# Kernel optimization log

Hardware: AMD Instinct MI355X
Metric: run time of the kernel (lower is better)

Reference implementation:

```python
import jax, jax.numpy as jnp
import numpy as np

B, M, H, E, V, U = 1024, 15, 256, 256, 30000, 1000


def setup_inputs() -> dict:
    key = jax.random.key(0)
    ks = jax.random.split(key, 24)
    s = 0.05  # weight init scale
    return {
        "input_ids": jax.random.randint(ks[0], (B, 1), 0, V),
        "input_embedding": jax.random.normal(ks[1], (B, 1, E), jnp.float32),
        "hidden": jax.random.normal(ks[2], (1, B, H), jnp.float32),
        "inter_output": jax.random.normal(ks[3], (B, M, H), jnp.float32),
        "user_list": jax.random.randint(ks[4], (B,), 0, U),
        # per-user parameter tables (torch ModuleLists of Linear); stored [in,out]
        "inter_W": jax.random.normal(ks[5], (U, H, H), jnp.float32) * s,
        "inter_b": jax.random.normal(ks[6], (U, H), jnp.float32) * s,
        "hidden_W": jax.random.normal(ks[7], (U, H, H), jnp.float32) * s,
        "hidden_b": jax.random.normal(ks[8], (U, H), jnp.float32) * s,
        "lt1_W": jax.random.normal(ks[9], (U, 2 * H, H), jnp.float32) * s,
        "lt1_b": jax.random.normal(ks[10], (U, H), jnp.float32) * s,
        "scale_W": jax.random.normal(ks[11], (U, H), jnp.float32) * s,
        "scale_b": jax.random.normal(ks[12], (U,), jnp.float32) * s,
        # GRU (1 layer), torch layout: W_ih [3H, 2E], W_hh [3H, H], gate order r,z,n
        "gru_Wih": jax.random.normal(ks[13], (3 * H, 2 * E), jnp.float32) * s,
        "gru_Whh": jax.random.normal(ks[14], (3 * H, H), jnp.float32) * s,
        "gru_bih": jax.random.normal(ks[15], (3 * H,), jnp.float32) * s,
        "gru_bhh": jax.random.normal(ks[16], (3 * H,), jnp.float32) * s,
        # output projection, stored [H, V]
        "lin_W": jax.random.normal(ks[17], (H, V), jnp.float32) * s,
        "lin_b": jax.random.normal(ks[18], (V,), jnp.float32) * s,
    }


def reference(input_ids, input_embedding, hidden, inter_output, user_list,
              inter_W, inter_b, hidden_W, hidden_b, lt1_W, lt1_b,
              scale_W, scale_b, gru_Wih, gru_Whh, gru_bih, gru_bhh,
              lin_W, lin_b):
    embedded_input = input_embedding  # dropout p=0 (eval)
    hidden_t = jnp.transpose(hidden, (1, 0, 2))  # [B,1,H]

    # per-user intra attention: gather user weights, batched GEMMs (replaces python loop)
    Wi = inter_W[user_list]                      # [B,H,H]
    inter_output_a = jnp.einsum('bmh,bho->bmo', inter_output, Wi) + inter_b[user_list][:, None, :]
    Wh = hidden_W[user_list]                     # [B,H,H]
    hidden_t_a = jnp.einsum('bih,bho->bio', hidden_t, Wh) + hidden_b[user_list][:, None, :]  # [B,1,H]
    cat = jnp.concatenate([jnp.broadcast_to(hidden_t_a, (hidden_t_a.shape[0], M, H)), inter_output_a], axis=2)  # [B,M,2H]
    result = jnp.tanh(jnp.einsum('bmk,bko->bmo', cat, lt1_W[user_list]) + lt1_b[user_list][:, None, :])  # [B,M,H]
    energies = jnp.einsum('bmh,bh->bm', result, scale_W[user_list]) + scale_b[user_list][:, None]  # [B,M]

    attn_weights = jax.nn.softmax(energies, axis=1)                      # [B,M]
    context = jnp.einsum('bm,bmh->bh', attn_weights, inter_output)[:, None, :]  # [B,1,H]

    gru_input = jnp.concatenate([embedded_input, context], axis=2)  # [B,1,2E]
    x = gru_input[:, 0, :]
    h = hidden[0]
    gi = x @ gru_Wih.T + gru_bih   # [B,3H]
    gh = h @ gru_Whh.T + gru_bhh
    gi_r, gi_z, gi_n = jnp.split(gi, 3, axis=1)
    gh_r, gh_z, gh_n = jnp.split(gh, 3, axis=1)
    r = jax.nn.sigmoid(gi_r + gh_r)
    z = jax.nn.sigmoid(gi_z + gh_z)
    n = jnp.tanh(gi_n + r * gh_n)
    h_new = (1.0 - z) * n + z * h
    gru_output = h_new[:, None, :]       # [B,1,H]
    hidden_new = h_new[None, :, :]       # [1,B,H]

    output = gru_output @ lin_W + lin_b  # [B,1,V]
    return (output, hidden_new, embedded_input, gru_output, attn_weights)
```

## Files before the change

### kernel.cpp

```cpp
#include <hip/hip_runtime.h>
#include <math.h>

#define B 1024
#define M 15
#define H 256
#define E 256
#define V 30000
#define U 1000

typedef float  vf4    __attribute__((ext_vector_type(4)));
typedef __bf16 bf16x8 __attribute__((ext_vector_type(8)));
typedef float  f32x4  __attribute__((ext_vector_type(4)));

#define O_OUT   0
#define O_HID   ((size_t)B*V)
#define O_EMB   (O_HID + (size_t)B*H)
#define O_GRU   (O_EMB + (size_t)B*E)
#define O_ATT   (O_GRU + (size_t)B*H)

#define GLDS(g, l) __builtin_amdgcn_global_load_lds( \
    (const __attribute__((address_space(1))) void*)(g), \
    (__attribute__((address_space(3))) void*)(l), 16, 0, 0)

union BF8 { __bf16 h[8]; bf16x8 v; };
union BF4 { __bf16 h[4]; unsigned long long u; };

__global__ __launch_bounds__(1024) void sort_kernel(
    const int* __restrict__ ul, int* __restrict__ order, int* __restrict__ rbase_g)
{
    __shared__ int cnt[1024];
    __shared__ int base[1024];
    const int tid = threadIdx.x;
    cnt[tid] = 0;
    __syncthreads();
    const int u = ul[tid];
    atomicAdd(&cnt[u], 1);
    __syncthreads();
    int c0 = cnt[tid];
    int v  = c0;
    for (int off = 1; off < 1024; off <<= 1) {
        int add = (tid >= off) ? cnt[tid - off] : 0;
        __syncthreads();
        v += add;
        cnt[tid] = v;
        __syncthreads();
    }
    base[tid]   = v - c0;
    rbase_g[tid] = v - c0;
    __syncthreads();
    int pos = atomicAdd(&base[u], 1);
    order[pos] = tid;
}

__global__ __launch_bounds__(256, 4) void attn_kernel(
    const float* __restrict__ hidden,
    const float* __restrict__ inter_output,
    const int*   __restrict__ user_list,
    const int*   __restrict__ order,
    const int*   __restrict__ rbase,
    const float* __restrict__ inter_W,
    const float* __restrict__ inter_b,
    const float* __restrict__ hidden_W,
    const float* __restrict__ hidden_b,
    const float* __restrict__ lt1_W,
    const float* __restrict__ lt1_b,
    const float* __restrict__ scale_W,
    const float* __restrict__ scale_b,
    float* __restrict__ out,
    __bf16* __restrict__ xcat)
{
    const int s   = ((blockIdx.x & 7) << 7) + (blockIdx.x >> 3);
    const int b0  = order[s];
    const int u   = user_list[b0];
    if ((s - rbase[u]) & 1) return;
    bool paired = false;
    int  b1 = b0;
    if (s + 1 < B) {
        int ob = order[s + 1];
        if (user_list[ob] == u) { paired = true; b1 = ob; }
    }

    const int tid  = threadIdx.x;
    const int lane = tid & 63;
    const int wave = tid >> 6;
    const int wn0  = wave * 64;

    __shared__ __align__(16) __bf16 Abuf[32 * 512];
    __shared__ __align__(16) __bf16 hta[2][256];
    __shared__ float red[2][64];
    __shared__ float e_lds[2][16];

    {
        const int r    = tid >> 3;
        const int part = tid & 7;
        const int sm   = r >> 4;
        const int mr   = r & 15;
        const int bs   = sm ? b1 : b0;
        const bool zr  = (sm == 1) && !paired;
        #pragma unroll
        for (int it = 0; it < 8; ++it) {
            int c = part + it * 8;
            int k = c * 8;
            BF8 p;
            #pragma unroll
            for (int j = 0; j < 8; ++j) p.h[j] = (__bf16)0.f;
            if (!zr) {
                if (mr < 15 && k < 256) {
                    vf4 f0 = *(const vf4*)&inter_output[(size_t)bs * M * H + mr * H + k];
                    vf4 f1 = *(const vf4*)&inter_output[(size_t)bs * M * H + mr * H + k + 4];
                    p.h[0]=(__bf16)f0[0]; p.h[1]=(__bf16)f0[1]; p.h[2]=(__bf16)f0[2]; p.h[3]=(__bf16)f0[3];
                    p.h[4]=(__bf16)f1[0]; p.h[5]=(__bf16)f1[1]; p.h[6]=(__bf16)f1[2]; p.h[7]=(__bf16)f1[3];
                } else if (mr == 15 && k >= 256) {
                    vf4 f0 = *(const vf4*)&hidden[(size_t)bs * H + (k - 256)];
                    vf4 f1 = *(const vf4*)&hidden[(size_t)bs * H + (k - 256) + 4];
                    p.h[0]=(__bf16)f0[0]; p.h[1]=(__bf16)f0[1]; p.h[2]=(__bf16)f0[2]; p.h[3]=(__bf16)f0[3];
                    p.h[4]=(__bf16)f1[0]; p.h[5]=(__bf16)f1[1]; p.h[6]=(__bf16)f1[2]; p.h[7]=(__bf16)f1[3];
                }
            }
            *(bf16x8*)&Abuf[r * 512 + (c ^ (r & 7)) * 8] = p.v;
        }
    }
    __syncthreads();

    const float* Wi_base  = inter_W  + (size_t)u * H * H;
    const float* Wh_base  = hidden_W + (size_t)u * H * H;
    const float* lt1_base = lt1_W    + (size_t)u * 2 * H * H;

    const int ocol = wn0 + (lane & 15);
    const int krow = (lane >> 4) * 8;

    f32x4 acc1[2][4];
    #pragma unroll
    for (int mf = 0; mf < 2; ++mf)
        #pragma unroll
        for (int nf = 0; nf < 4; ++nf) { f32x4 z = {0.f,0.f,0.f,0.f}; acc1[mf][nf] = z; }

    #pragma unroll 2
    for (int ks = 0; ks < 16; ++ks) {
        const float* Bp = ((ks < 8) ? (Wi_base + (size_t)(ks * 32) * H)
                                    : (Wh_base + (size_t)((ks - 8) * 32) * H))
                          + (size_t)krow * H + ocol;
        float t[4][8];
        #pragma unroll
        for (int j = 0; j < 8; ++j)
            #pragma unroll
            for (int nf = 0; nf < 4; ++nf)
                t[nf][j] = Bp[(size_t)j * H + nf * 16];
        bf16x8 bfr[4];
        #pragma unroll
        for (int nf = 0; nf < 4; ++nf) {
            BF8 pk;
            #pragma unroll
            for (int j = 0; j < 8; ++j) pk.h[j] = (__bf16)t[nf][j];
            bfr[nf] = pk.v;
        }
        int sca = ((ks * 4 + (lane >> 4)) ^ (lane & 7)) * 8;
        bf16x8 a0 = *(const bf16x8*)&Abuf[(lane & 15) * 512 + sca];
        #pragma unroll
        for (int nf = 0; nf < 4; ++nf)
            acc1[0][nf] = __builtin_amdgcn_mfma_f32_16x16x32_bf16(a0, bfr[nf], acc1[0][nf], 0, 0, 0);
        if (paired) {
            bf16x8 a1 = *(const bf16x8*)&Abuf[(16 + (lane & 15)) * 512 + sca];
            #pragma unroll
            for (int nf = 0; nf < 4; ++nf)
                acc1[1][nf] = __builtin_amdgcn_mfma_f32_16x16x32_bf16(a1, bfr[nf], acc1[1][nf], 0, 0, 0);
        }
    }
    __syncthreads();

    if ((lane >> 4) == 3) {
        #pragma unroll
        for (int nf = 0; nf < 4; ++nf) {
            int o = wn0 + nf * 16 + (lane & 15);
            float hb = hidden_b[(size_t)u * H + o];
            hta[0][o] = (__bf16)(acc1[0][nf][3] + hb);
            hta[1][o] = (__bf16)(acc1[1][nf][3] + hb);
        }
    }
    #pragma unroll
    for (int mf = 0; mf < 2; ++mf) {
        #pragma unroll
        for (int nf = 0; nf < 4; ++nf) {
            int o  = wn0 + nf * 16 + (lane & 15);
            float bi = inter_b[(size_t)u * H + o];
            int k  = 256 + o;
            #pragma unroll
            for (int j = 0; j < 4; ++j) {
                int r  = mf * 16 + (lane >> 4) * 4 + j;
                Abuf[r * 512 + ((k >> 3) ^ (r & 7)) * 8 + (k & 7)] = (__bf16)(acc1[mf][nf][j] + bi);
            }
        }
    }
    __syncthreads();

    {
        const int r    = tid >> 3;
        const int part = tid & 7;
        const int sm   = r >> 4;
        #pragma unroll
        for (int it = 0; it < 4; ++it) {
            int c = part + it * 8;
            bf16x8 hv = *(const bf16x8*)&hta[sm][c * 8];
            *(bf16x8*)&Abuf[r * 512 + (c ^ (r & 7)) * 8] = hv;
        }
    }
    __syncthreads();

    f32x4 acc2[2][4];
    #pragma unroll
    for (int mf = 0; mf < 2; ++mf)
        #pragma unroll
        for (int nf = 0; nf < 4; ++nf) { f32x4 z = {0.f,0.f,0.f,0.f}; acc2[mf][nf] = z; }

    #pragma unroll 2
    for (int ks = 0; ks < 16; ++ks) {
        const float* Bp = lt1_base + (size_t)(ks * 32) * H + (size_t)krow * H + ocol;
        float t[4][8];
        #pragma unroll
        for (int j = 0; j < 8; ++j)
            #pragma unroll
            for (int nf = 0; nf < 4; ++nf)
                t[nf][j] = Bp[(size_t)j * H + nf * 16];
        bf16x8 bfr[4];
        #pragma unroll
        for (int nf = 0; nf < 4; ++nf) {
            BF8 pk;
            #pragma unroll
            for (int j = 0; j < 8; ++j) pk.h[j] = (__bf16)t[nf][j];
            bfr[nf] = pk.v;
        }
        int sca = ((ks * 4 + (lane >> 4)) ^ (lane & 7)) * 8;
        bf16x8 a0 = *(const bf16x8*)&Abuf[(lane & 15) * 512 + sca];
        #pragma unroll
        for (int nf = 0; nf < 4; ++nf)
            acc2[0][nf] = __builtin_amdgcn_mfma_f32_16x16x32_bf16(a0, bfr[nf], acc2[0][nf], 0, 0, 0);
        if (paired) {
            bf16x8 a1 = *(const bf16x8*)&Abuf[(16 + (lane & 15)) * 512 + sca];
            #pragma unroll
            for (int nf = 0; nf < 4; ++nf)
                acc2[1][nf] = __builtin_amdgcn_mfma_f32_16x16x32_bf16(a1, bfr[nf], acc2[1][nf], 0, 0, 0);
        }
    }

    float p0[4] = {0.f,0.f,0.f,0.f};
    float p1[4] = {0.f,0.f,0.f,0.f};
    #pragma unroll
    for (int nf = 0; nf < 4; ++nf) {
        int o = wn0 + nf * 16 + (lane & 15);
        float l1b = lt1_b[(size_t)u * H + o];
        float sw  = scale_W[(size_t)u * H + o];
        #pragma unroll
        for (int j = 0; j < 4; ++j)
            p0[j] += tanhf(acc2[0][nf][j] + l1b) * sw;
        if (paired)
            #pragma unroll
            for (int j = 0; j < 4; ++j)
                p1[j] += tanhf(acc2[1][nf][j] + l1b) * sw;
    }
    #pragma unroll
    for (int j = 0; j < 4; ++j) {
        float v = p0[j];
        v += __shfl_xor(v, 1, 64); v += __shfl_xor(v, 2, 64);
        v += __shfl_xor(v, 4, 64); v += __shfl_xor(v, 8, 64);
        if ((lane & 15) == 0) red[0][wave * 16 + (lane >> 4) * 4 + j] = v;
        float w = p1[j];
        w += __shfl_xor(w, 1, 64); w += __shfl_xor(w, 2, 64);
        w += __shfl_xor(w, 4, 64); w += __shfl_xor(w, 8, 64);
        if ((lane & 15) == 0) red[1][wave * 16 + (lane >> 4) * 4 + j] = w;
    }
    __syncthreads();
    if (tid < 32) {
        int sm = tid >> 4, mm = tid & 15;
        e_lds[sm][mm] = red[sm][mm] + red[sm][16 + mm] + red[sm][32 + mm] + red[sm][48 + mm]
                      + scale_b[u];
    }
    __syncthreads();

    const int nsm = paired ? 2 : 1;
    for (int sm = 0; sm < nsm; ++sm) {
        const int bs = sm ? b1 : b0;
        float mx = -1e30f;
        #pragma unroll
        for (int m = 0; m < M; ++m) mx = fmaxf(mx, e_lds[sm][m]);
        float sum = 0.f;
        float aw[M];
        #pragma unroll
        for (int m = 0; m < M; ++m) { aw[m] = expf(e_lds[sm][m] - mx); sum += aw[m]; }
        float inv = 1.f / sum;
        if (tid < M) out[O_ATT + (size_t)bs * M + tid] = aw[tid] * inv;
        float ctx = 0.f;
        #pragma unroll
        for (int m = 0; m < M; ++m)
            ctx += aw[m] * inter_output[(size_t)bs * M * H + m * H + tid];
        xcat[(size_t)bs * 768 + 256 + tid] = (__bf16)(ctx * inv);
    }
}

__global__ __launch_bounds__(256) void cvt_xh_kernel(
    const float* __restrict__ emb, const float* __restrict__ hidden,
    __bf16* __restrict__ xcat, float* __restrict__ out)
{
    const int b = blockIdx.x, tid = threadIdx.x;
    float ev = emb[(size_t)b * E + tid];
    float hv = hidden[(size_t)b * H + tid];
    xcat[(size_t)b * 768 + tid]       = (__bf16)ev;
    xcat[(size_t)b * 768 + 512 + tid] = (__bf16)hv;
    out[O_EMB + (size_t)b * E + tid]  = ev;
}

__global__ __launch_bounds__(192) void wcat_kernel(
    const float* __restrict__ Wih, const float* __restrict__ Whh,
    __bf16* __restrict__ wcat)
{
    const int n = blockIdx.x;
    const int k = threadIdx.x * 4;
    vf4 v = {0.f, 0.f, 0.f, 0.f};
    if (n < 512) {
        v = (k < 512) ? *(const vf4*)&Wih[(size_t)n * 512 + k]
                      : *(const vf4*)&Whh[(size_t)n * 256 + (k - 512)];
    } else if (n < 768) {
        if (k < 512) v = *(const vf4*)&Wih[(size_t)n * 512 + k];
    } else {
        if (k >= 512) v = *(const vf4*)&Whh[(size_t)(n - 256) * 256 + (k - 512)];
    }
    BF4 p;
    p.h[0]=(__bf16)v[0]; p.h[1]=(__bf16)v[1]; p.h[2]=(__bf16)v[2]; p.h[3]=(__bf16)v[3];
    *(unsigned long long*)&wcat[(size_t)n * 768 + k] = p.u;
}

__global__ __launch_bounds__(256) void xgemm_kernel(
    const __bf16* __restrict__ xcat, const __bf16* __restrict__ wcat,
    float* __restrict__ gates)
{
    const int n0   = blockIdx.x * 256;
    const int m0   = blockIdx.y * 64;
    const int tid  = threadIdx.x;
    const int wave = tid >> 6, lane = tid & 63;
    const int wn0  = wave * 64;

    __shared__ __align__(16) __bf16 Al[64 * 64];
    __shared__ __align__(16) __bf16 Bl[256 * 64];

    f32x4 acc[4][4];
    #pragma unroll
    for (int mf = 0; mf < 4; ++mf)
        #pragma unroll
        for (int nf = 0; nf < 4; ++nf) { f32x4 z = {0.f,0.f,0.f,0.f}; acc[mf][nf] = z; }

    for (int ks = 0; ks < 12; ++ks) {
        #pragma unroll
        for (int r = 0; r < 2; ++r) {
            int L = r * 256 + tid;
            int m = L >> 3, c = L & 7;
            int sc = c ^ (m & 7);
            GLDS(xcat + (size_t)(m0 + m) * 768 + ks * 64 + sc * 8, &Al[(size_t)L * 8]);
        }
        #pragma unroll
        for (int r = 0; r < 8; ++r) {
            int L = r * 256 + tid;
            int n = L >> 3, c = L & 7;
            int sc = c ^ (n & 7);
            GLDS(wcat + (size_t)(n0 + n) * 768 + ks * 64 + sc * 8, &Bl[(size_t)L * 8]);
        }
        __syncthreads();
        #pragma unroll
        for (int kk = 0; kk < 2; ++kk) {
            bf16x8 af[4];
            #pragma unroll
            for (int mf = 0; mf < 4; ++mf) {
                int row = mf * 16 + (lane & 15);
                int c   = kk * 4 + (lane >> 4);
                af[mf] = *(const bf16x8*)&Al[row * 64 + (c ^ (row & 7)) * 8];
            }
            bf16x8 bfr[4];
            #pragma unroll
            for (int nf = 0; nf < 4; ++nf) {
                int col = wn0 + nf * 16 + (lane & 15);
                int c   = kk * 4 + (lane >> 4);
                bfr[nf] = *(const bf16x8*)&Bl[col * 64 + (c ^ (col & 7)) * 8];
            }
            #pragma unroll
            for (int mf = 0; mf < 4; ++mf)
                #pragma unroll
                for (int nf = 0; nf < 4; ++nf)
                    acc[mf][nf] = __builtin_amdgcn_mfma_f32_16x16x32_bf16(
                        af[mf], bfr[nf], acc[mf][nf], 0, 0, 0);
        }
        __syncthreads();
    }

    #pragma unroll
    for (int nf = 0; nf < 4; ++nf) {
        int n = n0 + wn0 + nf * 16 + (lane & 15);
        #pragma unroll
        for (int mf = 0; mf < 4; ++mf) {
            int rbase_ = m0 + mf * 16 + (lane >> 4) * 4;
            f32x4 a = acc[mf][nf];
            #pragma unroll
            for (int j = 0; j < 4; ++j)
                gates[(size_t)(rbase_ + j) * 1024 + n] = a[j];
        }
    }
}

__global__ __launch_bounds__(256) void gate_kernel(
    const float* __restrict__ gates,
    const float* __restrict__ hidden,
    const float* __restrict__ bih, const float* __restrict__ bhh,
    float* __restrict__ out, __bf16* __restrict__ hnb)
{
    const int b = blockIdx.x, j = threadIdx.x;
    const float* g = gates + (size_t)b * 1024;
    float rs  = g[j]       + bih[j]       + bhh[j];
    float zs  = g[256 + j] + bih[256 + j] + bhh[256 + j];
    float gin = g[512 + j] + bih[512 + j];
    float ghn = g[768 + j] + bhh[512 + j];
    float h   = hidden[(size_t)b * H + j];
    float r_  = 1.f / (1.f + expf(-rs));
    float z_  = 1.f / (1.f + expf(-zs));
    float n_  = tanhf(gin + r_ * ghn);
    float hn  = (1.f - z_) * n_ + z_ * h;
    out[O_HID + (size_t)b * H + j] = hn;
    out[O_GRU + (size_t)b * H + j] = hn;
    hnb[(size_t)b * H + j] = (__bf16)hn;
}

__global__ __launch_bounds__(256) void transpose_kernel(
    const float* __restrict__ lin_W, __bf16* __restrict__ WT)
{
    const int v0  = blockIdx.x * 240;
    const int k0  = blockIdx.y * 64;
    const int tid = threadIdx.x;
    const int lane = tid & 63, kq = tid >> 6;

    __shared__ __bf16 T[240 * 68];

    if (lane < 60) {
        #pragma unroll
        for (int i = 0; i < 4; ++i) {
            int kr = kq * 16 + i * 4;
            vf4 f0 = *(const vf4*)&lin_W[(size_t)(k0 + kr + 0) * V + v0 + lane * 4];
            vf4 f1 = *(const vf4*)&lin_W[(size_t)(k0 + kr + 1) * V + v0 + lane * 4];
            vf4 f2 = *(const vf4*)&lin_W[(size_t)(k0 + kr + 2) * V + v0 + lane * 4];
            vf4 f3 = *(const vf4*)&lin_W[(size_t)(k0 + kr + 3) * V + v0 + lane * 4];
            #pragma unroll
            for (int j = 0; j < 4; ++j) {
                BF4 pk;
                pk.h[0] = (__bf16)f0[j];
                pk.h[1] = (__bf16)f1[j];
                pk.h[2] = (__bf16)f2[j];
                pk.h[3] = (__bf16)f3[j];
                int v = lane * 4 + j;
                *(unsigned long long*)&T[v * 68 + kr] = pk.u;
            }
        }
    }
    __syncthreads();

    for (int r = 0; r < 15; ++r) {
        int L = r * 256 + tid;
        int v = L >> 4, c = L & 15;
        *(unsigned long long*)&WT[(size_t)(v0 + v) * H + k0 + c * 4] =
            *(const unsigned long long*)&T[v * 68 + c * 4];
    }
}

#define GBM 64
#define GBN 256
#define GBK 64
#define NTM 16
#define NWG ((117 + 1) * NTM)
__global__ __launch_bounds__(256) void out_mfma_kernel(
    const __bf16* __restrict__ hnb,
    const __bf16* __restrict__ WT,
    const float* __restrict__ lin_b,
    float* __restrict__ out)
{
    const int L  = blockIdx.x;
    const int s  = (L & 7) * (NWG / 8) + (L >> 3);
    const int nt = s >> 4, mt = s & 15;
    const int n0 = nt * GBN;
    const int m0 = mt * GBM;
    const int tid  = threadIdx.x;
    const int wave = tid >> 6, lane = tid & 63;

    __shared__ __bf16 Al[GBM * H];
    __shared__ __bf16 Bl[GBN * GBK];

    #pragma unroll
    for (int r = 0; r < 8; ++r) {
        int Li = r * 256 + tid;
        int m = Li >> 5;
        int c = Li & 31;
        int sc = c ^ (m & 7);
        GLDS(hnb + (size_t)(m0 + m) * H + sc * 8, &Al[(size_t)Li * 8]);
    }

    f32x4 acc[4][4];
    #pragma unroll
    for (int mf = 0; mf < 4; ++mf)
        #pragma unroll
        for (int nf = 0; nf < 4; ++nf) {
            f32x4 z = {0.f, 0.f, 0.f, 0.f};
            acc[mf][nf] = z;
        }

    const int wn0 = wave * 64;

    for (int ks = 0; ks < 4; ++ks) {
        #pragma unroll
        for (int r = 0; r < 8; ++r) {
            int Li = r * 256 + tid;
            int n = Li >> 3;
            int c = Li & 7;
            int sc = c ^ (n & 7);
            int nn = n0 + n; if (nn >= V) nn = V - 1;
            GLDS(WT + (size_t)nn * H + ks * GBK + sc * 8, &Bl[(size_t)Li * 8]);
        }
        __syncthreads();

        #pragma unroll
        for (int kk = 0; kk < 2; ++kk) {
            bf16x8 af[4];
            #pragma unroll
            for (int mf = 0; mf < 4; ++mf) {
                int row = mf * 16 + (lane & 15);
                int c   = ks * 8 + kk * 4 + (lane >> 4);
                int cs  = c ^ (row & 7);
                af[mf] = *(const bf16x8*)&Al[row * H + cs * 8];
            }
            bf16x8 bfr[4];
            #pragma unroll
            for (int nf = 0; nf < 4; ++nf) {
                int col = wn0 + nf * 16 + (lane & 15);
                int c   = kk * 4 + (lane >> 4);
                int cs  = c ^ (col & 7);
                bfr[nf] = *(const bf16x8*)&Bl[col * GBK + cs * 8];
            }
            #pragma unroll
            for (int mf = 0; mf < 4; ++mf)
                #pragma unroll
                for (int nf = 0; nf < 4; ++nf)
                    acc[mf][nf] = __builtin_amdgcn_mfma_f32_16x16x32_bf16(
                        af[mf], bfr[nf], acc[mf][nf], 0, 0, 0);
        }
        __syncthreads();
    }

    #pragma unroll
    for (int nf = 0; nf < 4; ++nf) {
        int v = n0 + wn0 + nf * 16 + (lane & 15);
        if (v < V) {
            float lb = lin_b[v];
            #pragma unroll
            for (int mf = 0; mf < 4; ++mf) {
                int rbase_ = m0 + mf * 16 + (lane >> 4) * 4;
                f32x4 a = acc[mf][nf];
                #pragma unroll
                for (int j = 0; j < 4; ++j)
                    out[(size_t)(rbase_ + j) * V + v] = a[j] + lb;
            }
        }
    }
}

extern "C" void kernel_launch(void* const* d_in, const int* in_sizes, int n_in,
                              void* d_out, int out_size, void* d_ws, size_t ws_size,
                              hipStream_t stream) {
    const float* emb    = (const float*)d_in[1];
    const float* hidden = (const float*)d_in[2];
    const float* io     = (const float*)d_in[3];
    const int*   ul     = (const int*)  d_in[4];
    const float* iW     = (const float*)d_in[5];
    const float* ib     = (const float*)d_in[6];
    const float* hW     = (const float*)d_in[7];
    const float* hb     = (const float*)d_in[8];
    const float* l1W    = (const float*)d_in[9];
    const float* l1b    = (const float*)d_in[10];
    const float* sW     = (const float*)d_in[11];
    const float* sb     = (const float*)d_in[12];
    const float* Wih    = (const float*)d_in[13];
    const float* Whh    = (const float*)d_in[14];
    const float* bih    = (const float*)d_in[15];
    const float* bhh    = (const float*)d_in[16];
    const float* lW     = (const float*)d_in[17];
    const float* lb     = (const float*)d_in[18];

    float* out = (float*)d_out;
    char* ws = (char*)d_ws;
    int*    order = (int*)ws;
    int*    rbase = (int*)(ws + 4096);
    __bf16* xcat  = (__bf16*)(ws + 8192);
    __bf16* wcat  = (__bf16*)(ws + 8192 + 1572864);
    float*  gates = (float*) (ws + 8192 + 2 * 1572864);
    __bf16* hnb   = (__bf16*)(ws + 8192 + 2 * 1572864 + 4194304);
    __bf16* WT    = (__bf16*)(ws + 8192 + 2 * 1572864 + 4194304 + 524288);

    sort_kernel<<<1, 1024, 0, stream>>>(ul, order, rbase);
    attn_kernel<<<B, 256, 0, stream>>>(hidden, io, ul, order, rbase, iW, ib, hW, hb,
                                       l1W, l1b, sW, sb, out, xcat);
    cvt_xh_kernel<<<B, 256, 0, stream>>>(emb, hidden, xcat, out);
    wcat_kernel<<<1024, 192, 0, stream>>>(Wih, Whh, wcat);
    xgemm_kernel<<<dim3(4, 16), 256, 0, stream>>>(xcat, wcat, gates);
    gate_kernel<<<B, 256, 0, stream>>>(gates, hidden, bih, bhh, out, hnb);
    transpose_kernel<<<dim3(125, 4), 256, 0, stream>>>(lW, WT);
    out_mfma_kernel<<<NWG, 256, 0, stream>>>(hnb, WT, lb, out);
}
```

Before: 253.6 us.

## Fuse preprocessing kernels, retile GRU gate GEMM, vectorize output stores via LDS

Merges the attention, embedding/hidden conversion, GRU weight concatenation and lin_W transpose into one heterogeneous launch, with blocks dispatched by block index range. This removes three launches and lets the independent work overlap. The xgemm kernel is retiled to 64x64 output tiles with K=128 steps, giving 256 workgroups instead of 64 to fill more CUs. The output GEMM epilogue stages accumulators through LDS so it can write coalesced float4 rows with the bias added. The fused kernel now carries a larger shared allocation for every block type, which may cut occupancy for the smaller tasks.

```diff
diff --git a/kernel.cpp b/kernel.cpp
--- a/kernel.cpp
+++ b/kernel.cpp
@@ -52,7 +52,12 @@
     order[pos] = tid;
 }
 
-__global__ __launch_bounds__(256, 4) void attn_kernel(
+#define FB_ATTN 1024
+#define FB_TR   500
+#define FB_WC   256
+#define FB_TOT  (FB_ATTN + FB_TR + FB_WC)
+
+__global__ __launch_bounds__(256, 4) void fused_pre_kernel(
     const float* __restrict__ hidden,
     const float* __restrict__ inter_output,
     const int*   __restrict__ user_list,
@@ -66,12 +71,91 @@
     const float* __restrict__ lt1_b,
     const float* __restrict__ scale_W,
     const float* __restrict__ scale_b,
+    const float* __restrict__ emb,
+    const float* __restrict__ Wih,
+    const float* __restrict__ Whh,
+    const float* __restrict__ lin_W,
     float* __restrict__ out,
-    __bf16* __restrict__ xcat)
+    __bf16* __restrict__ xcat,
+    __bf16* __restrict__ wcat,
+    __bf16* __restrict__ WT)
 {
-    const int s   = ((blockIdx.x & 7) << 7) + (blockIdx.x >> 3);
+    __shared__ __align__(16) char smem[34432];
+    const int bid = blockIdx.x;
+    const int tid = threadIdx.x;
+
+    if (bid >= FB_ATTN + FB_TR) {
+        const int wb   = bid - (FB_ATTN + FB_TR);
+        const int wave = tid >> 6, lane = tid & 63;
+        const int n    = wb * 4 + wave;
+        #pragma unroll
+        for (int i = 0; i < 3; ++i) {
+            int k = i * 256 + lane * 4;
+            vf4 v = {0.f, 0.f, 0.f, 0.f};
+            if (n < 512) {
+                v = (k < 512) ? *(const vf4*)&Wih[(size_t)n * 512 + k]
+                              : *(const vf4*)&Whh[(size_t)n * 256 + (k - 512)];
+            } else if (n < 768) {
+                if (k < 512) v = *(const vf4*)&Wih[(size_t)n * 512 + k];
+            } else {
+                if (k >= 512) v = *(const vf4*)&Whh[(size_t)(n - 256) * 256 + (k - 512)];
+            }
+            BF4 p;
+            p.h[0]=(__bf16)v[0]; p.h[1]=(__bf16)v[1]; p.h[2]=(__bf16)v[2]; p.h[3]=(__bf16)v[3];
+            *(unsigned long long*)&wcat[(size_t)n * 768 + k] = p.u;
+        }
+        return;
+    }
+
+    if (bid >= FB_ATTN) {
+        const int t   = bid - FB_ATTN;
+        const int v0  = (t % 125) * 240;
+        const int k0  = (t / 125) * 64;
+        const int lane = tid & 63, kq = tid >> 6;
+        __bf16* T = (__bf16*)smem;
+
+        if (lane < 60) {
+            #pragma unroll
+            for (int i = 0; i < 4; ++i) {
+                int kr = kq * 16 + i * 4;
+                vf4 f0 = *(const vf4*)&lin_W[(size_t)(k0 + kr + 0) * V + v0 + lane * 4];
+                vf4 f1 = *(const vf4*)&lin_W[(size_t)(k0 + kr + 1) * V + v0 + lane * 4];
+                vf4 f2 = *(const vf4*)&lin_W[(size_t)(k0 + kr + 2) * V + v0 + lane * 4];
+                vf4 f3 = *(const vf4*)&lin_W[(size_t)(k0 + kr + 3) * V + v0 + lane * 4];
+                #pragma unroll
+                for (int j = 0; j < 4; ++j) {
+                    BF4 pk;
+                    pk.h[0] = (__bf16)f0[j];
+                    pk.h[1] = (__bf16)f1[j];
+                    pk.h[2] = (__bf16)f2[j];
+                    pk.h[3] = (__bf16)f3[j];
+                    int v = lane * 4 + j;
+                    *(unsigned long long*)&T[v * 68 + kr] = pk.u;
+                }
+            }
+        }
+        __syncthreads();
+        for (int r = 0; r < 15; ++r) {
+            int L = r * 256 + tid;
+            int v = L >> 4, c = L & 15;
+            *(unsigned long long*)&WT[(size_t)(v0 + v) * H + k0 + c * 4] =
+                *(const unsigned long long*)&T[v * 68 + c * 4];
+        }
+        return;
+    }
+
+    const int s   = ((bid & 7) << 7) + (bid >> 3);
     const int b0  = order[s];
     const int u   = user_list[b0];
+
+    {
+        float ev = emb[(size_t)b0 * E + tid];
+        float hv = hidden[(size_t)b0 * H + tid];
+        xcat[(size_t)b0 * 768 + tid]       = (__bf16)ev;
+        xcat[(size_t)b0 * 768 + 512 + tid] = (__bf16)hv;
+        out[O_EMB + (size_t)b0 * E + tid]  = ev;
+    }
+
     if ((s - rbase[u]) & 1) return;
     bool paired = false;
     int  b1 = b0;
@@ -80,15 +164,14 @@
         if (user_list[ob] == u) { paired = true; b1 = ob; }
     }
 
-    const int tid  = threadIdx.x;
     const int lane = tid & 63;
     const int wave = tid >> 6;
     const int wn0  = wave * 64;
 
-    __shared__ __align__(16) __bf16 Abuf[32 * 512];
-    __shared__ __align__(16) __bf16 hta[2][256];
-    __shared__ float red[2][64];
-    __shared__ float e_lds[2][16];
+    __bf16* Abuf = (__bf16*)smem;
+    __bf16* hta  = (__bf16*)(smem + 32768);
+    float*  red  = (float*)(smem + 32768 + 1024);
+    float*  e_lds= (float*)(smem + 32768 + 1024 + 512);
 
     {
         const int r    = tid >> 3;
@@ -173,8 +256,8 @@
         for (int nf = 0; nf < 4; ++nf) {
             int o = wn0 + nf * 16 + (lane & 15);
             float hb = hidden_b[(size_t)u * H + o];
-            hta[0][o] = (__bf16)(acc1[0][nf][3] + hb);
-            hta[1][o] = (__bf16)(acc1[1][nf][3] + hb);
+            hta[o]       = (__bf16)(acc1[0][nf][3] + hb);
+            hta[256 + o] = (__bf16)(acc1[1][nf][3] + hb);
         }
     }
     #pragma unroll
@@ -200,7 +283,7 @@
         #pragma unroll
         for (int it = 0; it < 4; ++it) {
             int c = part + it * 8;
-            bf16x8 hv = *(const bf16x8*)&hta[sm][c * 8];
+            bf16x8 hv = *(const bf16x8*)&hta[sm * 256 + c * 8];
             *(bf16x8*)&Abuf[r * 512 + (c ^ (r & 7)) * 8] = hv;
         }
     }
@@ -262,17 +345,18 @@
         float v = p0[j];
         v += __shfl_xor(v, 1, 64); v += __shfl_xor(v, 2, 64);
         v += __shfl_xor(v, 4, 64); v += __shfl_xor(v, 8, 64);
-        if ((lane & 15) == 0) red[0][wave * 16 + (lane >> 4) * 4 + j] = v;
+        if ((lane & 15) == 0) red[0 * 64 + wave * 16 + (lane >> 4) * 4 + j] = v;
         float w = p1[j];
         w += __shfl_xor(w, 1, 64); w += __shfl_xor(w, 2, 64);
         w += __shfl_xor(w, 4, 64); w += __shfl_xor(w, 8, 64);
-        if ((lane & 15) == 0) red[1][wave * 16 + (lane >> 4) * 4 + j] = w;
+        if ((lane & 15) == 0) red[1 * 64 + wave * 16 + (lane >> 4) * 4 + j] = w;
     }
     __syncthreads();
     if (tid < 32) {
         int sm = tid >> 4, mm = tid & 15;
-        e_lds[sm][mm] = red[sm][mm] + red[sm][16 + mm] + red[sm][32 + mm] + red[sm][48 + mm]
-                      + scale_b[u];
+        e_lds[sm * 16 + mm] = red[sm * 64 + mm] + red[sm * 64 + 16 + mm]
+                            + red[sm * 64 + 32 + mm] + red[sm * 64 + 48 + mm]
+                            + scale_b[u];
     }
     __syncthreads();
 
@@ -281,11 +365,11 @@
         const int bs = sm ? b1 : b0;
         float mx = -1e30f;
         #pragma unroll
-        for (int m = 0; m < M; ++m) mx = fmaxf(mx, e_lds[sm][m]);
+        for (int m = 0; m < M; ++m) mx = fmaxf(mx, e_lds[sm * 16 + m]);
         float sum = 0.f;
         float aw[M];
         #pragma unroll
-        for (int m = 0; m < M; ++m) { aw[m] = expf(e_lds[sm][m] - mx); sum += aw[m]; }
+        for (int m = 0; m < M; ++m) { aw[m] = expf(e_lds[sm * 16 + m] - mx); sum += aw[m]; }
         float inv = 1.f / sum;
         if (tid < M) out[O_ATT + (size_t)bs * M + tid] = aw[tid] * inv;
         float ctx = 0.f;
@@ -294,95 +378,63 @@
             ctx += aw[m] * inter_output[(size_t)bs * M * H + m * H + tid];
         xcat[(size_t)bs * 768 + 256 + tid] = (__bf16)(ctx * inv);
     }
-}
-
-__global__ __launch_bounds__(256) void cvt_xh_kernel(
-    const float* __restrict__ emb, const float* __restrict__ hidden,
-    __bf16* __restrict__ xcat, float* __restrict__ out)
-{
-    const int b = blockIdx.x, tid = threadIdx.x;
-    float ev = emb[(size_t)b * E + tid];
-    float hv = hidden[(size_t)b * H + tid];
-    xcat[(size_t)b * 768 + tid]       = (__bf16)ev;
-    xcat[(size_t)b * 768 + 512 + tid] = (__bf16)hv;
-    out[O_EMB + (size_t)b * E + tid]  = ev;
-}
-
-__global__ __launch_bounds__(192) void wcat_kernel(
-    const float* __restrict__ Wih, const float* __restrict__ Whh,
-    __bf16* __restrict__ wcat)
-{
-    const int n = blockIdx.x;
-    const int k = threadIdx.x * 4;
-    vf4 v = {0.f, 0.f, 0.f, 0.f};
-    if (n < 512) {
-        v = (k < 512) ? *(const vf4*)&Wih[(size_t)n * 512 + k]
-                      : *(const vf4*)&Whh[(size_t)n * 256 + (k - 512)];
-    } else if (n < 768) {
-        if (k < 512) v = *(const vf4*)&Wih[(size_t)n * 512 + k];
-    } else {
-        if (k >= 512) v = *(const vf4*)&Whh[(size_t)(n - 256) * 256 + (k - 512)];
-    }
-    BF4 p;
-    p.h[0]=(__bf16)v[0]; p.h[1]=(__bf16)v[1]; p.h[2]=(__bf16)v[2]; p.h[3]=(__bf16)v[3];
-    *(unsigned long long*)&wcat[(size_t)n * 768 + k] = p.u;
 }
 
 __global__ __launch_bounds__(256) void xgemm_kernel(
     const __bf16* __restrict__ xcat, const __bf16* __restrict__ wcat,
     float* __restrict__ gates)
 {
-    const int n0   = blockIdx.x * 256;
+    const int n0   = blockIdx.x * 64;
     const int m0   = blockIdx.y * 64;
     const int tid  = threadIdx.x;
     const int wave = tid >> 6, lane = tid & 63;
-    const int wn0  = wave * 64;
-
-    __shared__ __align__(16) __bf16 Al[64 * 64];
-    __shared__ __align__(16) __bf16 Bl[256 * 64];
-
-    f32x4 acc[4][4];
-    #pragma unroll
-    for (int mf = 0; mf < 4; ++mf)
-        #pragma unroll
-        for (int nf = 0; nf < 4; ++nf) { f32x4 z = {0.f,0.f,0.f,0.f}; acc[mf][nf] = z; }
-
-    for (int ks = 0; ks < 12; ++ks) {
-        #pragma unroll
-        for (int r = 0; r < 2; ++r) {
+    const int wm   = wave >> 1, wn = wave & 1;
+
+    __shared__ __align__(16) __bf16 Al[64 * 128];
+    __shared__ __align__(16) __bf16 Bl[64 * 128];
+
+    f32x4 acc[2][2];
+    #pragma unroll
+    for (int mf = 0; mf < 2; ++mf)
+        #pragma unroll
+        for (int nf = 0; nf < 2; ++nf) { f32x4 z = {0.f,0.f,0.f,0.f}; acc[mf][nf] = z; }
+
+    for (int ks = 0; ks < 6; ++ks) {
+        #pragma unroll
+        for (int r = 0; r < 4; ++r) {
             int L = r * 256 + tid;
-            int m = L >> 3, c = L & 7;
-            int sc = c ^ (m & 7);
-            GLDS(xcat + (size_t)(m0 + m) * 768 + ks * 64 + sc * 8, &Al[(size_t)L * 8]);
-        }
-        #pragma unroll
-        for (int r = 0; r < 8; ++r) {
+            int row = L >> 4, c = L & 15;
+            int sc = c ^ (row & 7);
+            GLDS(xcat + (size_t)(m0 + row) * 768 + ks * 128 + sc * 8, &Al[(size_t)L * 8]);
+        }
+        #pragma unroll
+        for (int r = 0; r < 4; ++r) {
             int L = r * 256 + tid;
-            int n = L >> 3, c = L & 7;
-            int sc = c ^ (n & 7);
-            GLDS(wcat + (size_t)(n0 + n) * 768 + ks * 64 + sc * 8, &Bl[(size_t)L * 8]);
+            int row = L >> 4, c = L & 15;
+            int sc = c ^ (row & 7);
+            GLDS(wcat + (size_t)(n0 + row) * 768 + ks * 128 + sc * 8, &Bl[(size_t)L * 8]);
         }
         __syncthreads();
         #pragma unroll
-        for (int kk = 0; kk < 2; ++kk) {
-            bf16x8 af[4];
-            #pragma unroll
-            for (int mf = 0; mf < 4; ++mf) {
-                int row = mf * 16 + (lane & 15);
+        for (int kk = 0; kk < 4; ++kk) {
+            bf16x8 af[2];
+            #pragma unroll
+            for (int mf = 0; mf < 2; ++mf) {
+                int row = wm * 32 + mf * 16 + (lane & 15);
                 int c   = kk * 4 + (lane >> 4);
-                af[mf] = *(const bf16x8*)&Al[row * 64 + (c ^ (row & 7)) * 8];
-            }
-            bf16x8 bfr[4];
-            #pragma unroll
-            for (int nf = 0; nf < 4; ++nf) {
-                int col = wn0 + nf * 16 + (lane & 15);
+                af[mf] = *(const bf16x8*)&Al[row * 128 + (c ^ (row & 7)) * 8];
+            }
+            bf16x8 bfr[2];
+            #pragma unroll
+            for (int nf = 0; nf < 2; ++nf) {
+                int col = wn * 32 + nf * 16 + (lane & 15);
                 int c   = kk * 4 + (lane >> 4);
-                bfr[nf] = *(const bf16x8*)&Bl[col * 64 + (c ^ (col & 7)) * 8];
-            }
-            #pragma unroll
-            for (int mf = 0; mf < 4; ++mf)
+                bfr[nf] = *(const bf16x8*)&Bl[col * 128 + (c ^ (col & 7)) * 8];
+            }
+            #pragma unroll
+            for (int mf = 0; mf < 2; ++mf)
                 #pragma unroll
-                for (int nf = 0; nf < 4; ++nf)
+                for (int nf = 0; nf < 2; ++nf)
                     acc[mf][nf] = __builtin_amdgcn_mfma_f32_16x16x32_bf16(
                         af[mf], bfr[nf], acc[mf][nf], 0, 0, 0);
         }
@@ -390,15 +442,15 @@
     }
 
     #pragma unroll
-    for (int nf = 0; nf < 4; ++nf) {
-        int n = n0 + wn0 + nf * 16 + (lane & 15);
-        #pragma unroll
-        for (int mf = 0; mf < 4; ++mf) {
-            int rbase_ = m0 + mf * 16 + (lane >> 4) * 4;
+    for (int nf = 0; nf < 2; ++nf) {
+        int n = n0 + wn * 32 + nf * 16 + (lane & 15);
+        #pragma unroll
+        for (int mf = 0; mf < 2; ++mf) {
+            int rb = m0 + wm * 32 + mf * 16 + (lane >> 4) * 4;
             f32x4 a = acc[mf][nf];
             #pragma unroll
             for (int j = 0; j < 4; ++j)
-                gates[(size_t)(rbase_ + j) * 1024 + n] = a[j];
+                gates[(size_t)(rb + j) * 1024 + n] = a[j];
         }
     }
 }
@@ -425,46 +477,6 @@
     hnb[(size_t)b * H + j] = (__bf16)hn;
 }
 
-__global__ __launch_bounds__(256) void transpose_kernel(
-    const float* __restrict__ lin_W, __bf16* __restrict__ WT)
-{
-    const int v0  = blockIdx.x * 240;
-    const int k0  = blockIdx.y * 64;
-    const int tid = threadIdx.x;
-    const int lane = tid & 63, kq = tid >> 6;
-
-    __shared__ __bf16 T[240 * 68];
-
-    if (lane < 60) {
-        #pragma unroll
-        for (int i = 0; i < 4; ++i) {
-            int kr = kq * 16 + i * 4;
-            vf4 f0 = *(const vf4*)&lin_W[(size_t)(k0 + kr + 0) * V + v0 + lane * 4];
-            vf4 f1 = *(const vf4*)&lin_W[(size_t)(k0 + kr + 1) * V + v0 + lane * 4];
-            vf4 f2 = *(const vf4*)&lin_W[(size_t)(k0 + kr + 2) * V + v0 + lane * 4];
-            vf4 f3 = *(const vf4*)&lin_W[(size_t)(k0 + kr + 3) * V + v0 + lane * 4];
-            #pragma unroll
-            for (int j = 0; j < 4; ++j) {
-                BF4 pk;
-                pk.h[0] = (__bf16)f0[j];
-                pk.h[1] = (__bf16)f1[j];
-                pk.h[2] = (__bf16)f2[j];
-                pk.h[3] = (__bf16)f3[j];
-                int v = lane * 4 + j;
-                *(unsigned long long*)&T[v * 68 + kr] = pk.u;
-            }
-        }
-    }
-    __syncthreads();
-
-    for (int r = 0; r < 15; ++r) {
-        int L = r * 256 + tid;
-        int v = L >> 4, c = L & 15;
-        *(unsigned long long*)&WT[(size_t)(v0 + v) * H + k0 + c * 4] =
-            *(const unsigned long long*)&T[v * 68 + c * 4];
-    }
-}
-
 #define GBM 64
 #define GBN 256
 #define GBK 64
@@ -484,8 +496,9 @@
     const int tid  = threadIdx.x;
     const int wave = tid >> 6, lane = tid & 63;
 
-    __shared__ __bf16 Al[GBM * H];
-    __shared__ __bf16 Bl[GBN * GBK];
+    __shared__ __align__(16) char gsm[GBM * H * 2 + GBN * GBK * 2];
+    __bf16* Al = (__bf16*)gsm;
+    __bf16* Bl = (__bf16*)(gsm + GBM * H * 2);
 
     #pragma unroll
     for (int r = 0; r < 8; ++r) {
@@ -547,20 +560,27 @@
         __syncthreads();
     }
 
+    float* Cs = (float*)gsm;
     #pragma unroll
     for (int nf = 0; nf < 4; ++nf) {
-        int v = n0 + wn0 + nf * 16 + (lane & 15);
-        if (v < V) {
-            float lb = lin_b[v];
-            #pragma unroll
-            for (int mf = 0; mf < 4; ++mf) {
-                int rbase_ = m0 + mf * 16 + (lane >> 4) * 4;
-                f32x4 a = acc[mf][nf];
-                #pragma unroll
-                for (int j = 0; j < 4; ++j)
-                    out[(size_t)(rbase_ + j) * V + v] = a[j] + lb;
-            }
-        }
+        int col = wn0 + nf * 16 + (lane & 15);
+        #pragma unroll
+        for (int mf = 0; mf < 4; ++mf) {
+            #pragma unroll
+            for (int j = 0; j < 4; ++j)
+                Cs[(mf * 16 + (lane >> 4) * 4 + j) * 256 + col] = acc[mf][nf][j];
+        }
+    }
+    __syncthreads();
+
+    const bool nok = (n0 + lane * 4 + 3 < V);
+    f32x4 lb = {0.f, 0.f, 0.f, 0.f};
+    if (nok) lb = *(const f32x4*)&lin_b[n0 + lane * 4];
+    for (int r = wave; r < 64; r += 4) {
+        f32x4 c = *(const f32x4*)&Cs[r * 256 + lane * 4];
+        c += lb;
+        if (nok)
+            *(f32x4*)&out[(size_t)(m0 + r) * V + n0 + lane * 4] = c;
     }
 }
 
@@ -597,12 +617,10 @@
     __bf16* WT    = (__bf16*)(ws + 8192 + 2 * 1572864 + 4194304 + 524288);
 
     sort_kernel<<<1, 1024, 0, stream>>>(ul, order, rbase);
-    attn_kernel<<<B, 256, 0, stream>>>(hidden, io, ul, order, rbase, iW, ib, hW, hb,
-                                       l1W, l1b, sW, sb, out, xcat);
-    cvt_xh_kernel<<<B, 256, 0, stream>>>(emb, hidden, xcat, out);
-    wcat_kernel<<<1024, 192, 0, stream>>>(Wih, Whh, wcat);
-    xgemm_kernel<<<dim3(4, 16), 256, 0, stream>>>(xcat, wcat, gates);
+    fused_pre_kernel<<<FB_TOT, 256, 0, stream>>>(
+        hidden, io, ul, order, rbase, iW, ib, hW, hb, l1W, l1b, sW, sb,
+        emb, Wih, Whh, lW, out, xcat, wcat, WT);
+    xgemm_kernel<<<dim3(16, 16), 256, 0, stream>>>(xcat, wcat, gates);
     gate_kernel<<<B, 256, 0, stream>>>(gates, hidden, bih, bhh, out, hnb);
-    transpose_kernel<<<dim3(125, 4), 256, 0, stream>>>(lW, WT);
     out_mfma_kernel<<<NWG, 256, 0, stream>>>(hnb, WT, lb, out);
 }
```

After: 244.1 us. -3.8%, faster.
